# Optimization experiments

Measured on AMD Instinct MI355X. Metric: run time of the kernel, lower is better.

## Reference

```python
import jax, jax.numpy as jnp
import numpy as np

B, S, D, OUT, CLS = 131072, 14, 16, 128, 7
EPS = 1e-5
SCALING = 1.0


def _layer_norm(x, g, b):
    # torch LayerNorm over last dim, biased variance
    m = jnp.mean(x, axis=-1, keepdims=True)
    v = jnp.mean((x - m) ** 2, axis=-1, keepdims=True)
    return (x - m) * jax.lax.rsqrt(v + EPS) * g + b


def setup_inputs() -> dict:
    key = jax.random.key(0)
    ks = jax.random.split(key, 20)
    p = lambda k, shp: jax.random.normal(k, shp, dtype=jnp.float32) * 0.05
    inp = {
        "sample": jax.random.normal(ks[0], (B, S, D), dtype=jnp.float32),
        # affine LayerNorms on state(query)/stored(key)/pattern-projection(value) inputs
        "ln_q_g": jnp.ones((D,), jnp.float32), "ln_q_b": jnp.zeros((D,), jnp.float32),
        "ln_k_g": jnp.ones((D,), jnp.float32), "ln_k_b": jnp.zeros((D,), jnp.float32),
        "ln_v_g": jnp.ones((D,), jnp.float32), "ln_v_b": jnp.zeros((D,), jnp.float32),
        # Hopfield association core projections (num_heads=1, head_dim=16)
        "Wq": p(ks[1], (D, D)), "bq": p(ks[2], (D,)),
        "Wk": p(ks[3], (D, D)), "bk": p(ks[4], (D,)),
        "Wv": p(ks[5], (D, D)), "bv": p(ks[6], (D,)),
        # Hopfield output projection 16 -> 128
        "Wo": p(ks[7], (OUT, D)), "bo": p(ks[8], (OUT,)),
        # Linear_m: 14 -> 1
        "Wm": p(ks[9], (1, S)), "bm": p(ks[10], (1,)),
        # Linear_b: 128 -> 7
        "Wb": p(ks[11], (CLS, OUT)), "bb": p(ks[12], (CLS,)),
    }
    return inp


def reference(sample, ln_q_g, ln_q_b, ln_k_g, ln_k_b, ln_v_g, ln_v_b,
              Wq, bq, Wk, bk, Wv, bv, Wo, bo, Wm, bm, Wb, bb):
    # --- Hopfield self-association (single update step) ---
    q_in = _layer_norm(sample, ln_q_g, ln_q_b)   # state pattern
    k_in = _layer_norm(sample, ln_k_g, ln_k_b)   # stored pattern
    v_in = _layer_norm(sample, ln_v_g, ln_v_b)   # pattern projection
    Q = jnp.einsum('bsd,ed->bse', q_in, Wq) + bq  # (B,S,16)
    K = jnp.einsum('bsd,ed->bse', k_in, Wk) + bk
    V = jnp.einsum('bsd,ed->bse', v_in, Wv) + bv
    A = jax.nn.softmax(SCALING * jnp.einsum('bqd,bkd->bqk', Q, K), axis=-1)  # (B,S,S)
    O = jnp.einsum('bqk,bkd->bqd', A, V)          # (B,S,16)
    x = jnp.einsum('bsd,od->bso', O, Wo) + bo     # (B,S,128)
    # --- head: transpose, Linear_m over seq dim, transpose, Linear_b ---
    x = jnp.swapaxes(x, 1, 2)                     # (B,128,S)
    y = jnp.einsum('bos,ms->bom', x, Wm) + bm     # (B,128,1)
    y = jnp.swapaxes(y, 1, 2)                     # (B,1,128)
    z = jnp.einsum('bmo,co->bmc', y, Wb) + bb     # (B,1,7)
    return jax.nn.softmax(z, axis=-1)
```

## Files before the change

kernel.cpp:

```cpp
#include <hip/hip_runtime.h>


#define NBATCH 131072

typedef float    f32x4 __attribute__((ext_vector_type(4)));
typedef _Float16 f16x4 __attribute__((ext_vector_type(4)));
typedef __fp16   h16x2 __attribute__((ext_vector_type(2)));

#define ROR(x,N) __int_as_float(__builtin_amdgcn_update_dpp(0, __float_as_int(x), 0x120 + (N), 0xF, 0xF, false))

static __device__ __forceinline__ f16x4 cvt4(float a, float b, float c, float d) {
    union { f16x4 v; h16x2 h[2]; } u;
    u.h[0] = __builtin_amdgcn_cvt_pkrtz(a, b);
    u.h[1] = __builtin_amdgcn_cvt_pkrtz(c, d);
    return u.v;
}

static __device__ __forceinline__ f32x4 mfma16(f16x4 a, f16x4 b, f32x4 c) {
#if __has_builtin(__builtin_amdgcn_mfma_f32_16x16x16f16)
    return __builtin_amdgcn_mfma_f32_16x16x16f16(a, b, c, 0, 0, 0);
#else
    f32x4 d;
    asm("v_mfma_f32_16x16x16_f16 %0, %1, %2, %3" : "=v"(d) : "v"(a), "v"(b), "v"(c));
    return d;
#endif
}

__global__ __launch_bounds__(256) void hop_prep(
    const float* __restrict__ gq, const float* __restrict__ bq_ln,
    const float* __restrict__ gk,
    const float* __restrict__ gv, const float* __restrict__ bv_ln,
    const float* __restrict__ Wq, const float* __restrict__ bq,
    const float* __restrict__ Wk,
    const float* __restrict__ Wv, const float* __restrict__ bv,
    const float* __restrict__ Wo, const float* __restrict__ bo,
    const float* __restrict__ Wm, const float* __restrict__ bm,
    const float* __restrict__ Wb, const float* __restrict__ bb,
    float* __restrict__ ws)
{
    __shared__ float WqP[256], WkP[256], WvP[256];
    __shared__ float bqP[16], bvP[16], WcS[112];
    const int t = threadIdx.x;
    {
        const int d = t & 15;
        WqP[t] = Wq[t] * gq[d];
        WkP[t] = Wk[t] * gk[d];
        WvP[t] = Wv[t] * gv[d];
    }
    if (t < 16) {
        float a = bq[t], c = bv[t];
        for (int d = 0; d < 16; ++d) {
            a = fmaf(Wq[t*16+d], bq_ln[d], a);
            c = fmaf(Wv[t*16+d], bv_ln[d], c);
        }
        bqP[t] = a; bvP[t] = c;
    }
    if (t < 112) {
        const int c = t >> 4, e = t & 15;
        float s = 0.f;
        for (int o = 0; o < 128; ++o) s = fmaf(Wb[c*128+o], Wo[o*16+e], s);
        WcS[t] = s;
    }
    __syncthreads();
    {
        const int dd = t >> 4, d = t & 15;
        float m = 0.f;
        for (int e = 0; e < 16; ++e) m = fmaf(WqP[e*16+d], WkP[e*16+dd], m);
        ws[t] = m;
    }
    if (t < 16) {
        float rr = 0.f;
        for (int e = 0; e < 16; ++e) rr = fmaf(bqP[e], WkP[e*16+t], rr);
        ws[256 + t] = rr;
    }
    {
        const int c = t >> 4, d = t & 15;
        float s = 0.f;
        if (c < 7)
            for (int e = 0; e < 16; ++e) s = fmaf(WcS[c*16+e], WvP[e*16+d], s);
        ws[272 + t] = s;
    }
    if (t < 16) {
        float v = 0.f;
        if (t < 7) {
            float wmsum = 0.f;
            for (int s = 0; s < 14; ++s) wmsum += Wm[s];
            float s1 = 0.f;
            for (int e = 0; e < 16; ++e) s1 = fmaf(WcS[t*16+e], bvP[e], s1);
            float s2 = 0.f, s3 = 0.f;
            for (int o = 0; o < 128; ++o) { s2 = fmaf(Wb[t*128+o], bo[o], s2); s3 += Wb[t*128+o]; }
            v = wmsum*s1 + wmsum*s2 + bm[0]*s3 + bb[t];
        }
        ws[528 + t] = v;
        ws[544 + t] = (t < 14) ? Wm[t] : 0.0f;
    }
}

__global__ __launch_bounds__(256) void hop_main(const float* __restrict__ smp,
                                                const float* __restrict__ W,
                                                float* __restrict__ out)
{
    const int wid = (blockIdx.x * 256 + threadIdx.x) >> 6;
    const int l   = threadIdx.x & 63;
    const int col = l & 15;
    const int q   = l >> 4;
    const size_t gbase = (size_t)wid * 4;

    const float4 mt = *reinterpret_cast<const float4*>(W + col*16 + q*4);
    const float4 w2 = *reinterpret_cast<const float4*>(W + 272 + col*16 + q*4);
    const float4 r4 = *reinterpret_cast<const float4*>(W + 256 + q*4);
    const float wm_l = W[544 + col];
    const float c2_l = W[528 + col];
    const f16x4 mtA  = cvt4(mt.x, mt.y, mt.z, mt.w);
    const f16x4 w2B  = cvt4(w2.x, w2.y, w2.z, w2.w);
    const f16x4 ONE  = {(_Float16)1.0f, (_Float16)1.0f, (_Float16)1.0f, (_Float16)1.0f};
    const f16x4 SIXT = {(_Float16)0.0625f, (_Float16)0.0625f, (_Float16)0.0625f, (_Float16)0.0625f};
    const f32x4 zero = {0.f, 0.f, 0.f, 0.f};
    const f32x4 rC   = {r4.x, r4.y, r4.z, r4.w};
    const f32x4 c2C  = {c2_l, c2_l, c2_l, c2_l};
    const float L2E  = 1.4426950408889634f;

    const int srow = (col < 14) ? col : 13;
    const float* bp = smp + gbase * 224 + srow * 16 + q * 4;

    float zb0, zb1, zb2, zb3;
    #pragma unroll
    for (int bb = 0; bb < 4; ++bb) {
        const float4 x = *reinterpret_cast<const float4*>(bp + bb * 224);

        const f16x4 xf  = cvt4(x.x, x.y, x.z, x.w);
        const f16x4 xqf = cvt4(x.x*x.x, x.y*x.y, x.z*x.z, x.w*x.w);
        const f32x4 S1 = mfma16(SIXT, xf,  zero);
        const f32x4 S2 = mfma16(SIXT, xqf, zero);
        const float mean = S1[0];
        const float var  = fmaf(-mean, mean, S2[0]);
        const float rstd = __builtin_amdgcn_rsqf(var + 1e-5f);
        const float nmr  = -mean * rstd;
        const f16x4 xhA = cvt4(fmaf(x.x, rstd, nmr), fmaf(x.y, rstd, nmr),
                               fmaf(x.z, rstd, nmr), fmaf(x.w, rstd, nmr));

        const f32x4 P = mfma16(xhA, w2B, zero);
        const f32x4 T = mfma16(mtA, xhA, rC);
        const f16x4 B2 = cvt4(T[0], T[1], T[2], T[3]);
        const f32x4 SS = mfma16(xhA, B2, zero);

        const bool hi = (q == 3);
        const float e0 = __builtin_amdgcn_exp2f(SS[0] * L2E);
        const float e1 = __builtin_amdgcn_exp2f(SS[1] * L2E);
        float e2 = __builtin_amdgcn_exp2f(SS[2] * L2E);
        float e3 = __builtin_amdgcn_exp2f(SS[3] * L2E);
        e2 = hi ? 0.0f : e2;
        e3 = hi ? 0.0f : e3;

        const f16x4 Ef16 = cvt4(e0, e1, e2, e3);
        const f32x4 Zm = mfma16(ONE, Ef16, zero);
        const float f = wm_l * __builtin_amdgcn_rcpf(Zm[0]);

        const f16x4 EfA = cvt4(e0*f, e1*f, e2*f, e3*f);
        const f16x4 Pf  = cvt4(P[0], P[1], P[2], P[3]);
        const f32x4 G = mfma16(EfA, Pf, zero);

        const f16x4 Gf = cvt4(G[0], G[1], G[2], G[3]);
        const f32x4 ZZ = mfma16(ONE, Gf, c2C);
        const float zz = ZZ[0];

        if      (bb == 0) zb0 = zz;
        else if (bb == 1) zb1 = zz;
        else if (bb == 2) zb2 = zz;
        else              zb3 = zz;
    }

    float z = (q == 1) ? zb1 : zb0;
    z = (q == 2) ? zb2 : z;
    z = (q == 3) ? zb3 : z;
    float e = (col < 7) ? __builtin_amdgcn_exp2f(z * L2E) : 0.0f;
    float s = e;
    s += ROR(s, 1); s += ROR(s, 2); s += ROR(s, 4); s += ROR(s, 8);
    if (col < 7) out[(gbase + q) * 7 + col] = e * __builtin_amdgcn_rcpf(s);
}

extern "C" void kernel_launch(void* const* d_in, const int* in_sizes, int n_in,
                              void* d_out, int out_size, void* d_ws, size_t ws_size,
                              hipStream_t stream) {
    (void)in_sizes; (void)n_in; (void)out_size; (void)ws_size;
    const float* smp = (const float*)d_in[0];
    float* ws = (float*)d_ws;
    hop_prep<<<1, 256, 0, stream>>>(
        (const float*)d_in[1],  (const float*)d_in[2],
        (const float*)d_in[3],
        (const float*)d_in[5],  (const float*)d_in[6],
        (const float*)d_in[7],  (const float*)d_in[8],
        (const float*)d_in[9],
        (const float*)d_in[11], (const float*)d_in[12],
        (const float*)d_in[13], (const float*)d_in[14],
        (const float*)d_in[15], (const float*)d_in[16],
        (const float*)d_in[17], (const float*)d_in[18],
        ws);
    hop_main<<<NBATCH * 16 / 256, 256, 0, stream>>>(smp, ws, (float*)d_out);
}
```

Before: 36.14 us.

## Process four batch groups per wave with double-buffered prefetched loads

Each wave now handles four groups of four samples. It preloads the next group's inputs while computing the current one, and the grid shrinks by a factor of four. The log2(e) scaling is folded into the precomputed weights, which removes per-element multiplies. The softmax normalization is restructured so the row sums and the value products come from MFMAs that can be issued in parallel, and the reciprocal weights are folded into the final reduction MFMA. The cost is higher register pressure and fewer waves to hide memory latency.

```diff
diff --git a/kernel.cpp b/kernel.cpp
--- a/kernel.cpp
+++ b/kernel.cpp
@@ -2,6 +2,8 @@
 
 
 #define NBATCH 131072
+#define NWAVES 8192
+#define ITERF  ((size_t)NWAVES * 896)
 
 typedef float    f32x4 __attribute__((ext_vector_type(4)));
 typedef _Float16 f16x4 __attribute__((ext_vector_type(4)));
@@ -38,6 +40,7 @@
     const float* __restrict__ Wb, const float* __restrict__ bb,
     float* __restrict__ ws)
 {
+    const float L2E = 1.4426950408889634f;
     __shared__ float WqP[256], WkP[256], WvP[256];
     __shared__ float bqP[16], bvP[16], WcS[112];
     const int t = threadIdx.x;
@@ -66,12 +69,12 @@
         const int dd = t >> 4, d = t & 15;
         float m = 0.f;
         for (int e = 0; e < 16; ++e) m = fmaf(WqP[e*16+d], WkP[e*16+dd], m);
-        ws[t] = m;
+        ws[t] = m * L2E;
     }
     if (t < 16) {
         float rr = 0.f;
         for (int e = 0; e < 16; ++e) rr = fmaf(bqP[e], WkP[e*16+t], rr);
-        ws[256 + t] = rr;
+        ws[256 + t] = rr * L2E;
     }
     {
         const int c = t >> 4, d = t & 15;
@@ -91,26 +94,25 @@
             for (int o = 0; o < 128; ++o) { s2 = fmaf(Wb[t*128+o], bo[o], s2); s3 += Wb[t*128+o]; }
             v = wmsum*s1 + wmsum*s2 + bm[0]*s3 + bb[t];
         }
-        ws[528 + t] = v;
-        ws[544 + t] = (t < 14) ? Wm[t] : 0.0f;
-    }
-}
-
-__global__ __launch_bounds__(256) void hop_main(const float* __restrict__ smp,
-                                                const float* __restrict__ W,
-                                                float* __restrict__ out)
+        ws[528 + t] = v * L2E;
+        ws[544 + t] = (t < 14) ? Wm[t] * L2E : 0.0f;
+    }
+}
+
+__global__ __launch_bounds__(256, 4) void hop_main(const float* __restrict__ smp,
+                                                   const float* __restrict__ W,
+                                                   float* __restrict__ out)
 {
-    const int wid = (blockIdx.x * 256 + threadIdx.x) >> 6;
-    const int l   = threadIdx.x & 63;
-    const int col = l & 15;
-    const int q   = l >> 4;
-    const size_t gbase = (size_t)wid * 4;
-
-    const float4 mt = *reinterpret_cast<const float4*>(W + col*16 + q*4);
-    const float4 w2 = *reinterpret_cast<const float4*>(W + 272 + col*16 + q*4);
-    const float4 r4 = *reinterpret_cast<const float4*>(W + 256 + q*4);
-    const float wm_l = W[544 + col];
-    const float c2_l = W[528 + col];
+    const int wave = (blockIdx.x * 256 + threadIdx.x) >> 6;
+    const int l    = threadIdx.x & 63;
+    const int col  = l & 15;
+    const int q    = l >> 4;
+
+    const float4 mt  = *reinterpret_cast<const float4*>(W + col*16 + q*4);
+    const float4 w2  = *reinterpret_cast<const float4*>(W + 272 + col*16 + q*4);
+    const float4 r4  = *reinterpret_cast<const float4*>(W + 256 + q*4);
+    const float4 wm4 = *reinterpret_cast<const float4*>(W + 544 + q*4);
+    const float  c2_l = W[528 + col];
     const f16x4 mtA  = cvt4(mt.x, mt.y, mt.z, mt.w);
     const f16x4 w2B  = cvt4(w2.x, w2.y, w2.z, w2.w);
     const f16x4 ONE  = {(_Float16)1.0f, (_Float16)1.0f, (_Float16)1.0f, (_Float16)1.0f};
@@ -118,16 +120,14 @@
     const f32x4 zero = {0.f, 0.f, 0.f, 0.f};
     const f32x4 rC   = {r4.x, r4.y, r4.z, r4.w};
     const f32x4 c2C  = {c2_l, c2_l, c2_l, c2_l};
-    const float L2E  = 1.4426950408889634f;
+    const bool  hi   = (q == 3);
 
     const int srow = (col < 14) ? col : 13;
-    const float* bp = smp + gbase * 224 + srow * 16 + q * 4;
-
-    float zb0, zb1, zb2, zb3;
-    #pragma unroll
-    for (int bb = 0; bb < 4; ++bb) {
-        const float4 x = *reinterpret_cast<const float4*>(bp + bb * 224);
-
+    const float* p0 = smp + (size_t)wave * 896 + srow * 16 + q * 4;
+    float* op = out + ((size_t)wave * 4 + q) * 7 + col;
+    const size_t OSTEP = (size_t)NWAVES * 4 * 7;
+
+    auto zbatch = [&](const float4& x) -> float {
         const f16x4 xf  = cvt4(x.x, x.y, x.z, x.w);
         const f16x4 xqf = cvt4(x.x*x.x, x.y*x.y, x.z*x.z, x.w*x.w);
         const f32x4 S1 = mfma16(SIXT, xf,  zero);
@@ -138,45 +138,54 @@
         const float nmr  = -mean * rstd;
         const f16x4 xhA = cvt4(fmaf(x.x, rstd, nmr), fmaf(x.y, rstd, nmr),
                                fmaf(x.z, rstd, nmr), fmaf(x.w, rstd, nmr));
-
         const f32x4 P = mfma16(xhA, w2B, zero);
-        const f32x4 T = mfma16(mtA, xhA, rC);
+        const f32x4 T  = mfma16(mtA, xhA, rC);
         const f16x4 B2 = cvt4(T[0], T[1], T[2], T[3]);
         const f32x4 SS = mfma16(xhA, B2, zero);
-
-        const bool hi = (q == 3);
-        const float e0 = __builtin_amdgcn_exp2f(SS[0] * L2E);
-        const float e1 = __builtin_amdgcn_exp2f(SS[1] * L2E);
-        float e2 = __builtin_amdgcn_exp2f(SS[2] * L2E);
-        float e3 = __builtin_amdgcn_exp2f(SS[3] * L2E);
-        e2 = hi ? 0.0f : e2;
-        e3 = hi ? 0.0f : e3;
-
-        const f16x4 Ef16 = cvt4(e0, e1, e2, e3);
-        const f32x4 Zm = mfma16(ONE, Ef16, zero);
-        const float f = wm_l * __builtin_amdgcn_rcpf(Zm[0]);
-
-        const f16x4 EfA = cvt4(e0*f, e1*f, e2*f, e3*f);
-        const f16x4 Pf  = cvt4(P[0], P[1], P[2], P[3]);
-        const f32x4 G = mfma16(EfA, Pf, zero);
-
+        const float e0 = __builtin_amdgcn_exp2f(SS[0]);
+        const float e1 = __builtin_amdgcn_exp2f(SS[1]);
+        const float e2 = hi ? 0.0f : __builtin_amdgcn_exp2f(SS[2]);
+        const float e3 = hi ? 0.0f : __builtin_amdgcn_exp2f(SS[3]);
+        const f16x4 E  = cvt4(e0, e1, e2, e3);
+        const f16x4 Pf = cvt4(P[0], P[1], P[2], P[3]);
+        const f32x4 Zt = mfma16(E, ONE, zero);
+        const f32x4 G  = mfma16(E, Pf,  zero);
+        const float w0 = wm4.x * __builtin_amdgcn_rcpf(Zt[0]);
+        const float w1 = wm4.y * __builtin_amdgcn_rcpf(Zt[1]);
+        const float w2s = wm4.z * __builtin_amdgcn_rcpf(Zt[2]);
+        const float w3 = wm4.w * __builtin_amdgcn_rcpf(Zt[3]);
+        const f16x4 wA = cvt4(w0, w1, w2s, w3);
         const f16x4 Gf = cvt4(G[0], G[1], G[2], G[3]);
-        const f32x4 ZZ = mfma16(ONE, Gf, c2C);
-        const float zz = ZZ[0];
-
-        if      (bb == 0) zb0 = zz;
-        else if (bb == 1) zb1 = zz;
-        else if (bb == 2) zb2 = zz;
-        else              zb3 = zz;
-    }
-
-    float z = (q == 1) ? zb1 : zb0;
-    z = (q == 2) ? zb2 : z;
-    z = (q == 3) ? zb3 : z;
-    float e = (col < 7) ? __builtin_amdgcn_exp2f(z * L2E) : 0.0f;
-    float s = e;
-    s += ROR(s, 1); s += ROR(s, 2); s += ROR(s, 4); s += ROR(s, 8);
-    if (col < 7) out[(gbase + q) * 7 + col] = e * __builtin_amdgcn_rcpf(s);
+        const f32x4 ZZ = mfma16(wA, Gf, c2C);
+        return ZZ[0];
+    };
+
+    auto epilogue = [&](float z0, float z1, float z2, float z3, float* o) {
+        float z = (q == 1) ? z1 : z0;
+        z = (q == 2) ? z2 : z;
+        z = (q == 3) ? z3 : z;
+        float e = (col < 7) ? __builtin_amdgcn_exp2f(z) : 0.0f;
+        float s = e;
+        s += ROR(s, 1); s += ROR(s, 2); s += ROR(s, 4); s += ROR(s, 8);
+        if (col < 7) *o = e * __builtin_amdgcn_rcpf(s);
+    };
+
+#define LD4(v0, v1, v2, v3, it) { const float* pp = p0 + (size_t)(it) * ITERF; \
+    v0 = *reinterpret_cast<const float4*>(pp);        \
+    v1 = *reinterpret_cast<const float4*>(pp + 224);  \
+    v2 = *reinterpret_cast<const float4*>(pp + 448);  \
+    v3 = *reinterpret_cast<const float4*>(pp + 672); }
+
+    float4 a0, a1, a2, a3, b0, b1, b2, b3;
+    LD4(a0, a1, a2, a3, 0);
+    LD4(b0, b1, b2, b3, 1);
+    epilogue(zbatch(a0), zbatch(a1), zbatch(a2), zbatch(a3), op);
+    LD4(a0, a1, a2, a3, 2);
+    epilogue(zbatch(b0), zbatch(b1), zbatch(b2), zbatch(b3), op + OSTEP);
+    LD4(b0, b1, b2, b3, 3);
+    epilogue(zbatch(a0), zbatch(a1), zbatch(a2), zbatch(a3), op + 2*OSTEP);
+    epilogue(zbatch(b0), zbatch(b1), zbatch(b2), zbatch(b3), op + 3*OSTEP);
+#undef LD4
 }
 
 extern "C" void kernel_launch(void* const* d_in, const int* in_sizes, int n_in,
@@ -196,5 +205,5 @@
         (const float*)d_in[15], (const float*)d_in[16],
         (const float*)d_in[17], (const float*)d_in[18],
         ws);
-    hop_main<<<NBATCH * 16 / 256, 256, 0, stream>>>(smp, ws, (float*)d_out);
-}
+    hop_main<<<NWAVES * 64 / 256, 256, 0, stream>>>(smp, ws, (float*)d_out);
+}
```

Result: faster. 34.43 us (-4.7%).
